# Kernel tuning notes

Measured on AMD Instinct MI355X. Metric: run time of the kernel, lower is better.

The kernel has to match this reference:

```python
import jax, jax.numpy as jnp
import numpy as np

N = 50000
E = 800000
IN_DIM = 128
HIDDEN = 32
HEADS = 4
NUM_CLASSES = 10


def _glorot(key, shape):
    fan_in, fan_out = shape
    lim = float(np.sqrt(6.0 / (fan_in + fan_out)))
    return jax.random.uniform(key, shape, jnp.float32, -lim, lim)


def transformer_conv(x, src, dst, Wq, bq, Wk, bk, Wv, bv, Ws, bs, heads, out_ch, concat):
    """PyG TransformerConv (root_weight=True, beta=False, no edge_attr), eval mode."""
    n = x.shape[0]
    q = (x @ Wq + bq).reshape(n, heads, out_ch)
    k = (x @ Wk + bk).reshape(n, heads, out_ch)
    v = (x @ Wv + bv).reshape(n, heads, out_ch)
    # gather per-edge: query from target i, key/value from source j
    qe = q[dst]                                  # [E, H, C]
    ke = k[src]                                  # [E, H, C]
    ve = v[src]                                  # [E, H, C]
    logits = jnp.einsum('ehc,ehc->eh', qe, ke) / jnp.sqrt(jnp.float32(out_ch))
    # segment softmax over incoming edges of each target node
    m = jax.ops.segment_max(logits, dst, num_segments=n)        # [N, H]
    m = jnp.where(jnp.isfinite(m), m, 0.0)
    e = jnp.exp(logits - m[dst])                                # [E, H]
    denom = jax.ops.segment_sum(e, dst, num_segments=n)         # [N, H]
    alpha = e / (denom[dst] + 1e-16)                            # [E, H]
    agg = jax.ops.segment_sum(alpha[..., None] * ve, dst, num_segments=n)  # [N, H, C]
    if concat:
        out = agg.reshape(n, heads * out_ch)
    else:
        out = agg.mean(axis=1)
    return out + x @ Ws + bs  # root/skip connection


def setup_inputs() -> dict:
    key = jax.random.key(0)
    ks = jax.random.split(key, 20)
    x = jax.random.normal(ks[0], (N, IN_DIM), jnp.float32)
    edge_index = jax.random.randint(ks[1], (2, E), 0, N, jnp.int32)
    d1 = HEADS * HIDDEN  # conv1 per-head stacked width = 128
    params = {
        'Wq1': _glorot(ks[2], (IN_DIM, d1)), 'bq1': jnp.zeros((d1,), jnp.float32),
        'Wk1': _glorot(ks[3], (IN_DIM, d1)), 'bk1': jnp.zeros((d1,), jnp.float32),
        'Wv1': _glorot(ks[4], (IN_DIM, d1)), 'bv1': jnp.zeros((d1,), jnp.float32),
        'Ws1': _glorot(ks[5], (IN_DIM, d1)), 'bs1': jnp.zeros((d1,), jnp.float32),
        'Wq2': _glorot(ks[6], (d1, NUM_CLASSES)), 'bq2': jnp.zeros((NUM_CLASSES,), jnp.float32),
        'Wk2': _glorot(ks[7], (d1, NUM_CLASSES)), 'bk2': jnp.zeros((NUM_CLASSES,), jnp.float32),
        'Wv2': _glorot(ks[8], (d1, NUM_CLASSES)), 'bv2': jnp.zeros((NUM_CLASSES,), jnp.float32),
        'Ws2': _glorot(ks[9], (d1, NUM_CLASSES)), 'bs2': jnp.zeros((NUM_CLASSES,), jnp.float32),
    }
    return {'x': x, 'edge_index': edge_index, **params}


def reference(x, edge_index,
              Wq1, bq1, Wk1, bk1, Wv1, bv1, Ws1, bs1,
              Wq2, bq2, Wk2, bk2, Wv2, bv2, Ws2, bs2):
    src, dst = edge_index[0], edge_index[1]
    h = transformer_conv(x, src, dst, Wq1, bq1, Wk1, bk1, Wv1, bv1, Ws1, bs1,
                         HEADS, HIDDEN, concat=True)
    h = jax.nn.elu(h)
    # dropout is identity in eval mode
    out = transformer_conv(h, src, dst, Wq2, bq2, Wk2, bk2, Wv2, bv2, Ws2, bs2,
                           1, NUM_CLASSES, concat=False)
    return out
```

## Files before the change

kernel.cpp:

```cpp
#include <hip/hip_runtime.h>
#include <hip/hip_fp16.h>
#include <math.h>

#define NN 50000
#define EE 800000
#define NB 196
#define NBK 128
#define BKN 391
#define CH 4096

typedef _Float16 f16x8 __attribute__((ext_vector_type(8)));
typedef float f32x4 __attribute__((ext_vector_type(4)));
typedef float f32x2 __attribute__((ext_vector_type(2)));

__device__ inline float elu1(float x) { return x > 0.f ? x : expm1f(x); }

__global__ __launch_bounds__(256) void convert_x_deg(
    const float* __restrict__ x, __half* __restrict__ xh,
    const int* __restrict__ dst, int* __restrict__ deg)
{
    const int i = blockIdx.x * 256 + threadIdx.x;
    if (i < NN * 32) {
        const float4 v = ((const float4*)x)[i];
        ((__half2*)xh)[i * 2] = __floats2half2_rn(v.x, v.y);
        ((__half2*)xh)[i * 2 + 1] = __floats2half2_rn(v.z, v.w);
    }
    if (i < EE) atomicAdd(&deg[dst[i]], 1);
}

__global__ __launch_bounds__(256) void build_weights(
    const float* __restrict__ Wq, const float* __restrict__ Wk,
    const float* __restrict__ Wv, const float* __restrict__ Ws,
    const float* __restrict__ Wq2, const float* __restrict__ bq2,
    const float* __restrict__ Wk2, const float* __restrict__ bk2,
    const float* __restrict__ Wv2, const float* __restrict__ bv2,
    const float* __restrict__ Ws2, const float* __restrict__ bs2,
    __half* __restrict__ Wt, __half* __restrict__ W2t, float* __restrict__ bias2)
{
    const int idx = blockIdx.x * 256 + threadIdx.x;
    if (idx < 8192) {
        const int col = idx >> 7, k = idx & 127;
        const int m = col >> 4, j = col & 15;
        const float* W = m == 0 ? Wq2 : m == 1 ? Wk2 : m == 2 ? Wv2 : Ws2;
        W2t[idx] = (__half)(j < 10 ? W[k * 10 + j] : 0.f);
    }
    if (idx < 64) {
        const int m = idx >> 4, j = idx & 15;
        const float* b = m == 0 ? bq2 : m == 1 ? bk2 : m == 2 ? bv2 : bs2;
        bias2[idx] = j < 10 ? b[j] : 0.f;
    }
    __shared__ float tile[32][33];
    const int mat = blockIdx.x >> 4;
    const int tid = blockIdx.x & 15;
    const int k0 = (tid >> 2) * 32, c0 = (tid & 3) * 32;
    const float* W = mat == 0 ? Wq : mat == 1 ? Wk : mat == 2 ? Wv : Ws;
    const int r = threadIdx.x >> 5;
    const int c = threadIdx.x & 31;
    for (int rr = r; rr < 32; rr += 8) tile[rr][c] = W[(size_t)(k0 + rr) * 128 + c0 + c];
    __syncthreads();
    for (int rr = r; rr < 32; rr += 8)
        Wt[((size_t)mat * 128 + c0 + rr) * 128 + k0 + c] = (__half)tile[c][rr];
}

__global__ __launch_bounds__(256) void block_sums(
    const int* __restrict__ deg, int* __restrict__ bsum)
{
    __shared__ int ws[4];
    const int t = threadIdx.x;
    const int idx = blockIdx.x * 256 + t;
    int d = (idx < NN) ? deg[idx] : 0;
    #pragma unroll
    for (int off = 32; off; off >>= 1) d += __shfl_down(d, off, 64);
    if ((t & 63) == 0) ws[t >> 6] = d;
    __syncthreads();
    if (t == 0) bsum[blockIdx.x] = ws[0] + ws[1] + ws[2] + ws[3];
}

__global__ __launch_bounds__(256) void scan_bsums(int* __restrict__ bsum)
{
    __shared__ int s[256];
    const int t = threadIdx.x;
    int v = (t < NB) ? bsum[t] : 0;
    s[t] = v;
    __syncthreads();
    for (int off = 1; off < 256; off <<= 1) {
        int u = (t >= off) ? s[t - off] : 0;
        __syncthreads();
        s[t] += u;
        __syncthreads();
    }
    if (t < NB) bsum[t] = (t == 0) ? 0 : s[t - 1];
}

__global__ __launch_bounds__(256) void write_rowptr(
    const int* __restrict__ deg, const int* __restrict__ bsum,
    int* __restrict__ rowptr, int* __restrict__ bcur)
{
    __shared__ int s[256];
    const int t = threadIdx.x;
    const int idx = blockIdx.x * 256 + t;
    const int d = (idx < NN) ? deg[idx] : 0;
    s[t] = d;
    __syncthreads();
    for (int off = 1; off < 256; off <<= 1) {
        int u = (t >= off) ? s[t - off] : 0;
        __syncthreads();
        s[t] += u;
        __syncthreads();
    }
    const int excl = ((t == 0) ? 0 : s[t - 1]) + bsum[blockIdx.x];
    if (idx < NN) {
        rowptr[idx] = excl;
        if (idx % BKN == 0) bcur[idx / BKN] = excl;
    }
    if (idx == NN - 1) rowptr[NN] = excl + d;
}

__global__ __launch_bounds__(256) void bucket_stage(
    const int* __restrict__ src, const int* __restrict__ dst,
    int* __restrict__ bcur, unsigned* __restrict__ bpair)
{
    __shared__ unsigned ep[CH];
    __shared__ unsigned short eb[CH];
    __shared__ unsigned stg[CH];
    __shared__ int cnt[NBK], off[NBK], pos[NBK], gbase[NBK];
    const int t = threadIdx.x;
    const int e0 = blockIdx.x * CH;
    const int n = min(CH, EE - e0);
    if (t < NBK) cnt[t] = 0;
    __syncthreads();
    for (int i = t; i < n; i += 256) {
        const int s = src[e0 + i], d = dst[e0 + i];
        ep[i] = (unsigned)s | ((unsigned)d << 16);
        const int b = d / BKN;
        eb[i] = (unsigned short)b;
        atomicAdd(&cnt[b], 1);
    }
    __syncthreads();
    if (t == 0) {
        int run = 0;
        for (int b = 0; b < NBK; ++b) { off[b] = run; pos[b] = run; run += cnt[b]; }
    }
    __syncthreads();
    if (t < NBK && cnt[t] > 0) gbase[t] = atomicAdd(&bcur[t], cnt[t]);
    __syncthreads();
    for (int i = t; i < n; i += 256) {
        const int b = eb[i];
        const int p = atomicAdd(&pos[b], 1);
        stg[p] = ep[i];
    }
    __syncthreads();
    for (int i = t; i < n; i += 256) {
        int lo = 0, hi = NBK - 1;
        while (lo < hi) { const int mid = (lo + hi + 1) >> 1; if (off[mid] <= i) lo = mid; else hi = mid - 1; }
        bpair[gbase[lo] + (i - off[lo])] = stg[i];
    }
}

__global__ __launch_bounds__(256) void bucket_scatter(
    const unsigned* __restrict__ bpair, const int* __restrict__ rowptr,
    int* __restrict__ esrc)
{
    __shared__ int lcur[BKN];
    const int b = blockIdx.x;
    const int n0 = b * BKN;
    const int n1 = min(NN, n0 + BKN);
    const int nn = n1 - n0;
    const int t = threadIdx.x;
    for (int i = t; i < nn; i += 256) lcur[i] = rowptr[n0 + i];
    __syncthreads();
    const int ebeg = rowptr[n0];
    const int eend = rowptr[n1];
    for (int i = ebeg + t; i < eend; i += 256) {
        const unsigned p = bpair[i];
        const int s = (int)(p & 0xFFFFu);
        const int d = (int)(p >> 16);
        const int pos = atomicAdd(&lcur[d - n0], 1);
        esrc[pos] = s;
    }
}

__global__ __launch_bounds__(128) void gemm_l1_mfma(
    const __half* __restrict__ xh, const __half* __restrict__ Wt,
    const float* __restrict__ bq, const float* __restrict__ bk,
    const float* __restrict__ bv, const float* __restrict__ bs,
    __half* __restrict__ oqh, unsigned char* __restrict__ ok8,
    unsigned char* __restrict__ ov8, __half* __restrict__ osh)
{
    __shared__ __align__(16) unsigned char ldsraw[128 * 272];
    const int pair = blockIdx.y;
    const int t = threadIdx.x;
    const int wave = t >> 6;
    const int lane = t & 63;
    const int l = lane & 15;
    const int g = lane >> 4;
    const int brow0 = blockIdx.x * 128;
    const int wrow0 = brow0 + wave * 64;

    f16x8 xf[4][4];
    #pragma unroll
    for (int rt = 0; rt < 4; ++rt) {
        int arow = wrow0 + rt * 16 + l;
        if (arow >= NN) arow = NN - 1;
        #pragma unroll
        for (int kk = 0; kk < 4; ++kk)
            xf[rt][kk] = *(const f16x8*)((const _Float16*)xh + (size_t)arow * 128 + kk * 32 + g * 8);
    }

    for (int mi = 0; mi < 2; ++mi) {
        const int mat = pair * 2 + mi;
        const bool isfp8 = (mat == 1 || mat == 2);
        const float* b = mat == 0 ? bq : mat == 1 ? bk : mat == 2 ? bv : bs;
        const _Float16* wt = (const _Float16*)Wt + (size_t)mat * 128 * 128;

        f16x8 wf[4], wfn[4];
        #pragma unroll
        for (int kk = 0; kk < 4; ++kk)
            wf[kk] = *(const f16x8*)(wt + (size_t)l * 128 + kk * 32 + g * 8);

        for (int ct = 0; ct < 8; ++ct) {
            if (ct < 7) {
                const int ncol = (ct + 1) * 16 + l;
                #pragma unroll
                for (int kk = 0; kk < 4; ++kk)
                    wfn[kk] = *(const f16x8*)(wt + (size_t)ncol * 128 + kk * 32 + g * 8);
            }
            f32x4 acc[4];
            #pragma unroll
            for (int rt = 0; rt < 4; ++rt) acc[rt] = (f32x4){0.f, 0.f, 0.f, 0.f};
            #pragma unroll
            for (int kk = 0; kk < 4; ++kk)
                #pragma unroll
                for (int rt = 0; rt < 4; ++rt)
                    acc[rt] = __builtin_amdgcn_mfma_f32_16x16x32_f16(wf[kk], xf[rt][kk], acc[rt], 0, 0, 0);

            const int col0 = ct * 16 + g * 4;
            const float4 bias = *(const float4*)(b + col0);
            #pragma unroll
            for (int rt = 0; rt < 4; ++rt) {
                const int lrow = wave * 64 + rt * 16 + l;
                const float r0 = acc[rt][0] + bias.x;
                const float r1 = acc[rt][1] + bias.y;
                const float r2 = acc[rt][2] + bias.z;
                const float r3 = acc[rt][3] + bias.w;
                if (isfp8) {
                    int p = __builtin_amdgcn_cvt_pk_fp8_f32(r0, r1, 0, false);
                    p = __builtin_amdgcn_cvt_pk_fp8_f32(r2, r3, p, true);
                    *(int*)&ldsraw[lrow * 144 + col0] = p;
                } else {
                    __half2 h01 = __floats2half2_rn(r0, r1);
                    __half2 h23 = __floats2half2_rn(r2, r3);
                    uint2 u;
                    u.x = *(unsigned*)&h01;
                    u.y = *(unsigned*)&h23;
                    *(uint2*)&ldsraw[lrow * 272 + col0 * 2] = u;
                }
            }
            #pragma unroll
            for (int kk = 0; kk < 4; ++kk) wf[kk] = wfn[kk];
        }

        __syncthreads();
        if (isfp8) {
            unsigned char* o = (mat == 1) ? ok8 : ov8;
            #pragma unroll
            for (int i = 0; i < 8; ++i) {
                const int idx = i * 128 + t;
                const int row = idx >> 3;
                const int seg = idx & 7;
                const int grow = brow0 + row;
                if (grow < NN)
                    *(uint4*)(o + (size_t)grow * 128 + seg * 16) = *(const uint4*)&ldsraw[row * 144 + seg * 16];
            }
        } else {
            __half* o = (mat == 0) ? oqh : osh;
            #pragma unroll
            for (int i = 0; i < 16; ++i) {
                const int idx = i * 128 + t;
                const int row = idx >> 4;
                const int seg = idx & 15;
                const int grow = brow0 + row;
                if (grow < NN)
                    *(uint4*)(o + (size_t)grow * 128 + seg * 8) = *(const uint4*)&ldsraw[row * 272 + seg * 16];
            }
        }
        __syncthreads();
    }
}

__global__ __launch_bounds__(256) void node_attn1(
    const __half* __restrict__ q1, const unsigned char* __restrict__ k8,
    const unsigned char* __restrict__ v8,
    const int* __restrict__ rowptr, const int* __restrict__ esrc,
    const __half* __restrict__ skiph,
    __half* __restrict__ hb)
{
    const int t = threadIdx.x;
    const int d = blockIdx.x * 8 + (t >> 5);
    if (d >= NN) return;
    const int ch4 = (t & 31) << 2;

    const int beg = rowptr[d];
    const int end = rowptr[d + 1];

    float q0, q1v, q2, q3;
    {
        const __half2 qa = *(const __half2*)(q1 + (size_t)d * 128 + ch4);
        const __half2 qb = *(const __half2*)(q1 + (size_t)d * 128 + ch4 + 2);
        const float2 fa = __half22float2(qa);
        const float2 fb = __half22float2(qb);
        q0 = fa.x * 0.17677669529663687f;
        q1v = fa.y * 0.17677669529663687f;
        q2 = fb.x * 0.17677669529663687f;
        q3 = fb.y * 0.17677669529663687f;
    }

    f32x4 accA = {0.f, 0.f, 0.f, 0.f}, accB = {0.f, 0.f, 0.f, 0.f};
    float sA = 0.f, sB = 0.f;

    int i = beg;
    int sa = (i < end) ? esrc[i] : 0;
    int sb = (i + 1 < end) ? esrc[i + 1] : 0;
    unsigned kA = *(const unsigned*)(k8 + (size_t)sa * 128 + ch4);
    unsigned vA = *(const unsigned*)(v8 + (size_t)sa * 128 + ch4);
    unsigned kB = *(const unsigned*)(k8 + (size_t)sb * 128 + ch4);
    unsigned vB = *(const unsigned*)(v8 + (size_t)sb * 128 + ch4);

    while (i + 1 < end) {
        const int ni = i + 2;
        const int nsa = (ni < end) ? esrc[ni] : 0;
        const int nsb = (ni + 1 < end) ? esrc[ni + 1] : 0;
        const unsigned nkA = *(const unsigned*)(k8 + (size_t)nsa * 128 + ch4);
        const unsigned nvA = *(const unsigned*)(v8 + (size_t)nsa * 128 + ch4);
        const unsigned nkB = *(const unsigned*)(k8 + (size_t)nsb * 128 + ch4);
        const unsigned nvB = *(const unsigned*)(v8 + (size_t)nsb * 128 + ch4);

        const f32x2 kA01 = __builtin_amdgcn_cvt_pk_f32_fp8((int)kA, false);
        const f32x2 kA23 = __builtin_amdgcn_cvt_pk_f32_fp8((int)kA, true);
        const f32x2 kB01 = __builtin_amdgcn_cvt_pk_f32_fp8((int)kB, false);
        const f32x2 kB23 = __builtin_amdgcn_cvt_pk_f32_fp8((int)kB, true);

        float pA = q0 * kA01[0] + q1v * kA01[1] + q2 * kA23[0] + q3 * kA23[1];
        float pB = q0 * kB01[0] + q1v * kB01[1] + q2 * kB23[0] + q3 * kB23[1];
        pA += __shfl_xor(pA, 4, 8); pB += __shfl_xor(pB, 4, 8);
        pA += __shfl_xor(pA, 2, 8); pB += __shfl_xor(pB, 2, 8);
        pA += __shfl_xor(pA, 1, 8); pB += __shfl_xor(pB, 1, 8);

        const f32x2 vA01 = __builtin_amdgcn_cvt_pk_f32_fp8((int)vA, false);
        const f32x2 vA23 = __builtin_amdgcn_cvt_pk_f32_fp8((int)vA, true);
        const f32x2 vB01 = __builtin_amdgcn_cvt_pk_f32_fp8((int)vB, false);
        const f32x2 vB23 = __builtin_amdgcn_cvt_pk_f32_fp8((int)vB, true);

        const float exA = __expf(pA - 4.0f);
        accA[0] += exA * vA01[0];
        accA[1] += exA * vA01[1];
        accA[2] += exA * vA23[0];
        accA[3] += exA * vA23[1];
        sA += exA;

        const float exB = __expf(pB - 4.0f);
        accB[0] += exB * vB01[0];
        accB[1] += exB * vB01[1];
        accB[2] += exB * vB23[0];
        accB[3] += exB * vB23[1];
        sB += exB;

        kA = nkA; vA = nvA; kB = nkB; vB = nvB;
        i = ni;
    }
    if (i < end) {
        const f32x2 kA01 = __builtin_amdgcn_cvt_pk_f32_fp8((int)kA, false);
        const f32x2 kA23 = __builtin_amdgcn_cvt_pk_f32_fp8((int)kA, true);
        float pA = q0 * kA01[0] + q1v * kA01[1] + q2 * kA23[0] + q3 * kA23[1];
        pA += __shfl_xor(pA, 4, 8);
        pA += __shfl_xor(pA, 2, 8);
        pA += __shfl_xor(pA, 1, 8);
        const f32x2 vA01 = __builtin_amdgcn_cvt_pk_f32_fp8((int)vA, false);
        const f32x2 vA23 = __builtin_amdgcn_cvt_pk_f32_fp8((int)vA, true);
        const float exA = __expf(pA - 4.0f);
        accA[0] += exA * vA01[0];
        accA[1] += exA * vA01[1];
        accA[2] += exA * vA23[0];
        accA[3] += exA * vA23[1];
        sA += exA;
    }

    const float inv = 1.f / (sA + sB + 1e-16f);
    const __half2 sk01 = *(const __half2*)(skiph + (size_t)d * 128 + ch4);
    const __half2 sk23 = *(const __half2*)(skiph + (size_t)d * 128 + ch4 + 2);
    const float2 s01 = __half22float2(sk01);
    const float2 s23 = __half22float2(sk23);
    const float o0 = elu1(s01.x + (accA[0] + accB[0]) * inv);
    const float o1 = elu1(s01.y + (accA[1] + accB[1]) * inv);
    const float o2 = elu1(s23.x + (accA[2] + accB[2]) * inv);
    const float o3 = elu1(s23.y + (accA[3] + accB[3]) * inv);
    __half2 h01 = __floats2half2_rn(o0, o1);
    __half2 h23 = __floats2half2_rn(o2, o3);
    uint2 u;
    u.x = *(unsigned*)&h01;
    u.y = *(unsigned*)&h23;
    *(uint2*)(hb + (size_t)d * 128 + ch4) = u;
}

__global__ __launch_bounds__(128) void node_l2_mfma(
    const __half* __restrict__ hb, const __half* __restrict__ W2t,
    const float* __restrict__ bias2,
    __half* __restrict__ q2h, __half* __restrict__ kv2h,
    float* __restrict__ out)
{
    const int t = threadIdx.x;
    const int wave = t >> 6;
    const int lane = t & 63;
    const int l = lane & 15;
    const int g = lane >> 4;
    const int wrow0 = blockIdx.x * 128 + wave * 64;
    if (wrow0 >= NN) return;
    const bool full = (wrow0 + 64 <= NN);

    f16x8 hf[4][4];
    #pragma unroll
    for (int rt = 0; rt < 4; ++rt) {
        int arow = wrow0 + rt * 16 + l;
        if (!full && arow >= NN) arow = NN - 1;
        #pragma unroll
        for (int kk = 0; kk < 4; ++kk)
            hf[rt][kk] = *(const f16x8*)((const _Float16*)hb + (size_t)arow * 128 + kk * 32 + g * 8);
    }

    #pragma unroll
    for (int ct = 0; ct < 4; ++ct) {
        const int col = ct * 16 + l;
        f16x8 wf[4];
        #pragma unroll
        for (int kk = 0; kk < 4; ++kk)
            wf[kk] = *(const f16x8*)((const _Float16*)W2t + (size_t)col * 128 + kk * 32 + g * 8);

        f32x4 acc[4];
        #pragma unroll
        for (int rt = 0; rt < 4; ++rt) acc[rt] = (f32x4){0.f, 0.f, 0.f, 0.f};
        #pragma unroll
        for (int kk = 0; kk < 4; ++kk)
            #pragma unroll
            for (int rt = 0; rt < 4; ++rt)
                acc[rt] = __builtin_amdgcn_mfma_f32_16x16x32_f16(wf[kk], hf[rt][kk], acc[rt], 0, 0, 0);

        const int c0 = g * 4;
        const float4 bias = *(const float4*)(bias2 + ct * 16 + c0);
        #pragma unroll
        for (int rt = 0; rt < 4; ++rt) {
            const int row = wrow0 + rt * 16 + l;
            if (full || row < NN) {
                float4 r;
                r.x = acc[rt][0] + bias.x;
                r.y = acc[rt][1] + bias.y;
                r.z = acc[rt][2] + bias.z;
                r.w = acc[rt][3] + bias.w;
                if (ct == 3) {
                    if (g < 2) {
                        *(float4*)(out + (size_t)row * 10 + c0) = r;
                    } else if (g == 2) {
                        out[(size_t)row * 10 + 8] = r.x;
                        out[(size_t)row * 10 + 9] = r.y;
                    }
                } else {
                    __half* p = ct == 0 ? q2h + (size_t)row * 16 + c0
                              : kv2h + (size_t)row * 32 + (ct == 2 ? 16 : 0) + c0;
                    __half2 h01 = __floats2half2_rn(r.x, r.y);
                    __half2 h23 = __floats2half2_rn(r.z, r.w);
                    uint2 u;
                    u.x = *(unsigned*)&h01;
                    u.y = *(unsigned*)&h23;
                    *(uint2*)p = u;
                }
            }
        }
    }
}

__global__ __launch_bounds__(256) void node_attn2(
    const __half* __restrict__ q2h, const __half* __restrict__ kv2h,
    const int* __restrict__ rowptr, const int* __restrict__ esrc,
    float* __restrict__ out)
{
    const int t = threadIdx.x;
    const int d = blockIdx.x * 32 + (t >> 3);
    if (d >= NN) return;
    const int c = t & 7;
    const int beg = rowptr[d];
    const int end = rowptr[d + 1];

    float2 qv = __half22float2(*(const __half2*)(q2h + (size_t)d * 16 + 2 * c));
    qv.x *= 0.31622776601683794f;
    qv.y *= 0.31622776601683794f;

    float2 acc[4];
    float ss[4];
    #pragma unroll
    for (int j = 0; j < 4; ++j) { acc[j] = make_float2(0.f, 0.f); ss[j] = 0.f; }

    int i = beg;
    __half2 kr[4], vr[4];
    #pragma unroll
    for (int j = 0; j < 4; ++j) {
        const int s = (i + j < end) ? esrc[i + j] : 0;
        kr[j] = *(const __half2*)(kv2h + (size_t)s * 32 + 2 * c);
        vr[j] = *(const __half2*)(kv2h + (size_t)s * 32 + 16 + 2 * c);
    }

    while (i + 3 < end) {
        const int ni = i + 4;
        __half2 nk[4], nv[4];
        #pragma unroll
        for (int j = 0; j < 4; ++j) {
            const int s = (ni + j < end) ? esrc[ni + j] : 0;
            nk[j] = *(const __half2*)(kv2h + (size_t)s * 32 + 2 * c);
            nv[j] = *(const __half2*)(kv2h + (size_t)s * 32 + 16 + 2 * c);
        }
        #pragma unroll
        for (int j = 0; j < 4; ++j) {
            const float2 kf = __half22float2(kr[j]);
            const float2 vf = __half22float2(vr[j]);
            float p = qv.x * kf.x + qv.y * kf.y;
            p += __shfl_xor(p, 4, 8);
            p += __shfl_xor(p, 2, 8);
            p += __shfl_xor(p, 1, 8);
            const float ex = __expf(p - 2.0f);
            acc[j].x += ex * vf.x;
            acc[j].y += ex * vf.y;
            ss[j] += ex;
        }
        #pragma unroll
        for (int j = 0; j < 4; ++j) { kr[j] = nk[j]; vr[j] = nv[j]; }
        i = ni;
    }
    for (; i < end; ++i) {
        const int s = esrc[i];
        const float2 kf = __half22float2(*(const __half2*)(kv2h + (size_t)s * 32 + 2 * c));
        const float2 vf = __half22float2(*(const __half2*)(kv2h + (size_t)s * 32 + 16 + 2 * c));
        float p = qv.x * kf.x + qv.y * kf.y;
        p += __shfl_xor(p, 4, 8);
        p += __shfl_xor(p, 2, 8);
        p += __shfl_xor(p, 1, 8);
        const float ex = __expf(p - 2.0f);
        acc[0].x += ex * vf.x;
        acc[0].y += ex * vf.y;
        ss[0] += ex;
    }

    if (c < 5) {
        const float ssum = ss[0] + ss[1] + ss[2] + ss[3];
        const float inv = 1.f / (ssum + 1e-16f);
        float2 o = *(float2*)(out + (size_t)d * 10 + 2 * c);
        o.x += (acc[0].x + acc[1].x + acc[2].x + acc[3].x) * inv;
        o.y += (acc[0].y + acc[1].y + acc[2].y + acc[3].y) * inv;
        *(float2*)(out + (size_t)d * 10 + 2 * c) = o;
    }
}

extern "C" void kernel_launch(void* const* d_in, const int* in_sizes, int n_in,
                              void* d_out, int out_size, void* d_ws, size_t ws_size,
                              hipStream_t stream) {
    const float* x   = (const float*)d_in[0];
    const int*   ei  = (const int*)d_in[1];
    const float* Wq1 = (const float*)d_in[2];  const float* bq1 = (const float*)d_in[3];
    const float* Wk1 = (const float*)d_in[4];  const float* bk1 = (const float*)d_in[5];
    const float* Wv1 = (const float*)d_in[6];  const float* bv1 = (const float*)d_in[7];
    const float* Ws1 = (const float*)d_in[8];  const float* bs1 = (const float*)d_in[9];
    const float* Wq2 = (const float*)d_in[10]; const float* bq2 = (const float*)d_in[11];
    const float* Wk2 = (const float*)d_in[12]; const float* bk2 = (const float*)d_in[13];
    const float* Wv2 = (const float*)d_in[14]; const float* bv2 = (const float*)d_in[15];
    const float* Ws2 = (const float*)d_in[16]; const float* bs2 = (const float*)d_in[17];
    float* out = (float*)d_out;

    const int* src = ei;
    const int* dst = ei + EE;

    __half* xh    = (__half*)d_ws;
    __half* q1h   = xh + (size_t)NN * 128;
    __half* skiph = q1h + (size_t)NN * 128;
    __half* hb    = skiph + (size_t)NN * 128;
    unsigned char* k8 = (unsigned char*)(hb + (size_t)NN * 128);
    unsigned char* v8 = k8 + (size_t)NN * 128;
    __half* Wt    = (__half*)(v8 + (size_t)NN * 128);
    __half* W2t   = Wt + 4 * 128 * 128;
    __half* q2h   = W2t + 64 * 128;
    __half* kv2h  = q2h + (size_t)NN * 16;
    float* bias2  = (float*)(kv2h + (size_t)NN * 32);
    int* deg      = (int*)(bias2 + 64);
    int* rowptr   = deg + NN;
    int* bcur     = rowptr + NN + 1;
    int* bsum     = bcur + NBK;
    int* esrc     = bsum + NB;
    unsigned* bpair = (unsigned*)(esrc + EE);

    hipMemsetAsync(deg, 0, (size_t)NN * sizeof(int), stream);
    convert_x_deg<<<(NN * 32 + 255) / 256, 256, 0, stream>>>(x, xh, dst, deg);
    build_weights<<<64, 256, 0, stream>>>(Wq1, Wk1, Wv1, Ws1,
                                          Wq2, bq2, Wk2, bk2, Wv2, bv2, Ws2, bs2,
                                          Wt, W2t, bias2);

    block_sums<<<NB, 256, 0, stream>>>(deg, bsum);
    scan_bsums<<<1, 256, 0, stream>>>(bsum);
    write_rowptr<<<NB, 256, 0, stream>>>(deg, bsum, rowptr, bcur);
    bucket_stage<<<(EE + CH - 1) / CH, 256, 0, stream>>>(src, dst, bcur, bpair);
    bucket_scatter<<<NBK, 256, 0, stream>>>(bpair, rowptr, esrc);

    gemm_l1_mfma<<<dim3((NN + 127) / 128, 2), 128, 0, stream>>>(
        xh, Wt, bq1, bk1, bv1, bs1, q1h, k8, v8, skiph);

    node_attn1<<<(NN + 7) / 8, 256, 0, stream>>>(q1h, k8, v8, rowptr, esrc, skiph, hb);

    node_l2_mfma<<<(NN + 127) / 128, 128, 0, stream>>>(hb, W2t, bias2, q2h, kv2h, out);

    node_attn2<<<(NN + 31) / 32, 256, 0, stream>>>(q2h, kv2h, rowptr, esrc, out);
}
```

Baseline: 186.6 us.

## Rebalance layer-1 GEMM to 4 waves and narrow layer-2 attention to 4 lanes per node

The layer-1 projection GEMM now runs 256 threads per block, with each wave covering 32 rows instead of 64. This halves per-wave register use for the x fragments and accumulators, trading it for more weight-fragment reloads per row. The layer-2 attention kernel now assigns 4 lanes per destination node instead of 8, with each lane handling 4 channels via 8-byte loads. It processes two edges per iteration with prefetch, which reduces shuffle steps and idle lanes. The node_l2 output stores are also rewritten as float2 stores for alignment, since the 10-float row stride breaks float4 alignment.

After: 202.9 us. 8.7% more time.

```diff
diff --git a/kernel.cpp b/kernel.cpp
--- a/kernel.cpp
+++ b/kernel.cpp
@@ -180,7 +180,7 @@
     }
 }
 
-__global__ __launch_bounds__(128) void gemm_l1_mfma(
+__global__ __launch_bounds__(256) void gemm_l1_mfma(
     const __half* __restrict__ xh, const __half* __restrict__ Wt,
     const float* __restrict__ bq, const float* __restrict__ bk,
     const float* __restrict__ bv, const float* __restrict__ bs,
@@ -195,11 +195,11 @@
     const int l = lane & 15;
     const int g = lane >> 4;
     const int brow0 = blockIdx.x * 128;
-    const int wrow0 = brow0 + wave * 64;
-
-    f16x8 xf[4][4];
+    const int wrow0 = brow0 + wave * 32;
+
+    f16x8 xf[2][4];
     #pragma unroll
-    for (int rt = 0; rt < 4; ++rt) {
+    for (int rt = 0; rt < 2; ++rt) {
         int arow = wrow0 + rt * 16 + l;
         if (arow >= NN) arow = NN - 1;
         #pragma unroll
@@ -225,20 +225,20 @@
                 for (int kk = 0; kk < 4; ++kk)
                     wfn[kk] = *(const f16x8*)(wt + (size_t)ncol * 128 + kk * 32 + g * 8);
             }
-            f32x4 acc[4];
+            f32x4 acc[2];
             #pragma unroll
-            for (int rt = 0; rt < 4; ++rt) acc[rt] = (f32x4){0.f, 0.f, 0.f, 0.f};
+            for (int rt = 0; rt < 2; ++rt) acc[rt] = (f32x4){0.f, 0.f, 0.f, 0.f};
             #pragma unroll
             for (int kk = 0; kk < 4; ++kk)
                 #pragma unroll
-                for (int rt = 0; rt < 4; ++rt)
+                for (int rt = 0; rt < 2; ++rt)
                     acc[rt] = __builtin_amdgcn_mfma_f32_16x16x32_f16(wf[kk], xf[rt][kk], acc[rt], 0, 0, 0);
 
             const int col0 = ct * 16 + g * 4;
             const float4 bias = *(const float4*)(b + col0);
             #pragma unroll
-            for (int rt = 0; rt < 4; ++rt) {
-                const int lrow = wave * 64 + rt * 16 + l;
+            for (int rt = 0; rt < 2; ++rt) {
+                const int lrow = wave * 32 + rt * 16 + l;
                 const float r0 = acc[rt][0] + bias.x;
                 const float r1 = acc[rt][1] + bias.y;
                 const float r2 = acc[rt][2] + bias.z;
@@ -264,8 +264,8 @@
         if (isfp8) {
             unsigned char* o = (mat == 1) ? ok8 : ov8;
             #pragma unroll
-            for (int i = 0; i < 8; ++i) {
-                const int idx = i * 128 + t;
+            for (int i = 0; i < 4; ++i) {
+                const int idx = i * 256 + t;
                 const int row = idx >> 3;
                 const int seg = idx & 7;
                 const int grow = brow0 + row;
@@ -275,8 +275,8 @@
         } else {
             __half* o = (mat == 0) ? oqh : osh;
             #pragma unroll
-            for (int i = 0; i < 16; ++i) {
-                const int idx = i * 128 + t;
+            for (int i = 0; i < 8; ++i) {
+                const int idx = i * 256 + t;
                 const int row = idx >> 4;
                 const int seg = idx & 15;
                 const int grow = brow0 + row;
@@ -457,10 +457,10 @@
                 r.w = acc[rt][3] + bias.w;
                 if (ct == 3) {
                     if (g < 2) {
-                        *(float4*)(out + (size_t)row * 10 + c0) = r;
+                        *(float2*)(out + (size_t)row * 10 + c0) = make_float2(r.x, r.y);
+                        *(float2*)(out + (size_t)row * 10 + c0 + 2) = make_float2(r.z, r.w);
                     } else if (g == 2) {
-                        out[(size_t)row * 10 + 8] = r.x;
-                        out[(size_t)row * 10 + 9] = r.y;
+                        *(float2*)(out + (size_t)row * 10 + 8) = make_float2(r.x, r.y);
                     }
                 } else {
                     __half* p = ct == 0 ? q2h + (size_t)row * 16 + c0
@@ -483,77 +483,108 @@
     float* __restrict__ out)
 {
     const int t = threadIdx.x;
-    const int d = blockIdx.x * 32 + (t >> 3);
+    const int d = blockIdx.x * 64 + (t >> 2);
     if (d >= NN) return;
-    const int c = t & 7;
+    const int c = t & 3;
+    const int ch4 = c << 2;
     const int beg = rowptr[d];
     const int end = rowptr[d + 1];
 
-    float2 qv = __half22float2(*(const __half2*)(q2h + (size_t)d * 16 + 2 * c));
-    qv.x *= 0.31622776601683794f;
-    qv.y *= 0.31622776601683794f;
-
-    float2 acc[4];
-    float ss[4];
-    #pragma unroll
-    for (int j = 0; j < 4; ++j) { acc[j] = make_float2(0.f, 0.f); ss[j] = 0.f; }
+    float q0, q1v, q2v, q3v;
+    {
+        const __half2 qa = *(const __half2*)(q2h + (size_t)d * 16 + ch4);
+        const __half2 qb = *(const __half2*)(q2h + (size_t)d * 16 + ch4 + 2);
+        const float2 fa = __half22float2(qa);
+        const float2 fb = __half22float2(qb);
+        q0 = fa.x * 0.31622776601683794f;
+        q1v = fa.y * 0.31622776601683794f;
+        q2v = fb.x * 0.31622776601683794f;
+        q3v = fb.y * 0.31622776601683794f;
+    }
+
+    f32x4 accA = {0.f, 0.f, 0.f, 0.f}, accB = {0.f, 0.f, 0.f, 0.f};
+    float sA = 0.f, sB = 0.f;
 
     int i = beg;
-    __half2 kr[4], vr[4];
-    #pragma unroll
-    for (int j = 0; j < 4; ++j) {
-        const int s = (i + j < end) ? esrc[i + j] : 0;
-        kr[j] = *(const __half2*)(kv2h + (size_t)s * 32 + 2 * c);
-        vr[j] = *(const __half2*)(kv2h + (size_t)s * 32 + 16 + 2 * c);
-    }
-
-    while (i + 3 < end) {
-        const int ni = i + 4;
-        __half2 nk[4], nv[4];
-        #pragma unroll
-        for (int j = 0; j < 4; ++j) {
-            const int s = (ni + j < end) ? esrc[ni + j] : 0;
-            nk[j] = *(const __half2*)(kv2h + (size_t)s * 32 + 2 * c);
-            nv[j] = *(const __half2*)(kv2h + (size_t)s * 32 + 16 + 2 * c);
-        }
-        #pragma unroll
-        for (int j = 0; j < 4; ++j) {
-            const float2 kf = __half22float2(kr[j]);
-            const float2 vf = __half22float2(vr[j]);
-            float p = qv.x * kf.x + qv.y * kf.y;
-            p += __shfl_xor(p, 4, 8);
-            p += __shfl_xor(p, 2, 8);
-            p += __shfl_xor(p, 1, 8);
-            const float ex = __expf(p - 2.0f);
-            acc[j].x += ex * vf.x;
-            acc[j].y += ex * vf.y;
-            ss[j] += ex;
-        }
-        #pragma unroll
-        for (int j = 0; j < 4; ++j) { kr[j] = nk[j]; vr[j] = nv[j]; }
+    int sa = (i < end) ? esrc[i] : 0;
+    int sb = (i + 1 < end) ? esrc[i + 1] : 0;
+    uint2 kA = *(const uint2*)(kv2h + (size_t)sa * 32 + ch4);
+    uint2 vA = *(const uint2*)(kv2h + (size_t)sa * 32 + 16 + ch4);
+    uint2 kB = *(const uint2*)(kv2h + (size_t)sb * 32 + ch4);
+    uint2 vB = *(const uint2*)(kv2h + (size_t)sb * 32 + 16 + ch4);
+
+    while (i + 1 < end) {
+        const int ni = i + 2;
+        const int nsa = (ni < end) ? esrc[ni] : 0;
+        const int nsb = (ni + 1 < end) ? esrc[ni + 1] : 0;
+        const uint2 nkA = *(const uint2*)(kv2h + (size_t)nsa * 32 + ch4);
+        const uint2 nvA = *(const uint2*)(kv2h + (size_t)nsa * 32 + 16 + ch4);
+        const uint2 nkB = *(const uint2*)(kv2h + (size_t)nsb * 32 + ch4);
+        const uint2 nvB = *(const uint2*)(kv2h + (size_t)nsb * 32 + 16 + ch4);
+
+        const float2 kA01 = __half22float2(*(const __half2*)&kA.x);
+        const float2 kA23 = __half22float2(*(const __half2*)&kA.y);
+        const float2 kB01 = __half22float2(*(const __half2*)&kB.x);
+        const float2 kB23 = __half22float2(*(const __half2*)&kB.y);
+
+        float pA = q0 * kA01.x + q1v * kA01.y + q2v * kA23.x + q3v * kA23.y;
+        float pB = q0 * kB01.x + q1v * kB01.y + q2v * kB23.x + q3v * kB23.y;
+        pA += __shfl_xor(pA, 2, 4); pB += __shfl_xor(pB, 2, 4);
+        pA += __shfl_xor(pA, 1, 4); pB += __shfl_xor(pB, 1, 4);
+
+        const float2 vA01 = __half22float2(*(const __half2*)&vA.x);
+        const float2 vA23 = __half22float2(*(const __half2*)&vA.y);
+        const float2 vB01 = __half22float2(*(const __half2*)&vB.x);
+        const float2 vB23 = __half22float2(*(const __half2*)&vB.y);
+
+        const float exA = __expf(pA - 2.0f);
+        accA[0] += exA * vA01.x;
+        accA[1] += exA * vA01.y;
+        accA[2] += exA * vA23.x;
+        accA[3] += exA * vA23.y;
+        sA += exA;
+
+        const float exB = __expf(pB - 2.0f);
+        accB[0] += exB * vB01.x;
+        accB[1] += exB * vB01.y;
+        accB[2] += exB * vB23.x;
+        accB[3] += exB * vB23.y;
+        sB += exB;
+
+        kA = nkA; vA = nvA; kB = nkB; vB = nvB;
         i = ni;
     }
-    for (; i < end; ++i) {
-        const int s = esrc[i];
-        const float2 kf = __half22float2(*(const __half2*)(kv2h + (size_t)s * 32 + 2 * c));
-        const float2 vf = __half22float2(*(const __half2*)(kv2h + (size_t)s * 32 + 16 + 2 * c));
-        float p = qv.x * kf.x + qv.y * kf.y;
-        p += __shfl_xor(p, 4, 8);
-        p += __shfl_xor(p, 2, 8);
-        p += __shfl_xor(p, 1, 8);
-        const float ex = __expf(p - 2.0f);
-        acc[0].x += ex * vf.x;
-        acc[0].y += ex * vf.y;
-        ss[0] += ex;
-    }
-
-    if (c < 5) {
-        const float ssum = ss[0] + ss[1] + ss[2] + ss[3];
-        const float inv = 1.f / (ssum + 1e-16f);
-        float2 o = *(float2*)(out + (size_t)d * 10 + 2 * c);
-        o.x += (acc[0].x + acc[1].x + acc[2].x + acc[3].x) * inv;
-        o.y += (acc[0].y + acc[1].y + acc[2].y + acc[3].y) * inv;
-        *(float2*)(out + (size_t)d * 10 + 2 * c) = o;
+    if (i < end) {
+        const float2 kA01 = __half22float2(*(const __half2*)&kA.x);
+        const float2 kA23 = __half22float2(*(const __half2*)&kA.y);
+        float pA = q0 * kA01.x + q1v * kA01.y + q2v * kA23.x + q3v * kA23.y;
+        pA += __shfl_xor(pA, 2, 4);
+        pA += __shfl_xor(pA, 1, 4);
+        const float2 vA01 = __half22float2(*(const __half2*)&vA.x);
+        const float2 vA23 = __half22float2(*(const __half2*)&vA.y);
+        const float exA = __expf(pA - 2.0f);
+        accA[0] += exA * vA01.x;
+        accA[1] += exA * vA01.y;
+        accA[2] += exA * vA23.x;
+        accA[3] += exA * vA23.y;
+        sA += exA;
+    }
+
+    const float inv = 1.f / (sA + sB + 1e-16f);
+    if (c < 2) {
+        float2 o0 = *(float2*)(out + (size_t)d * 10 + ch4);
+        float2 o1 = *(float2*)(out + (size_t)d * 10 + ch4 + 2);
+        o0.x += (accA[0] + accB[0]) * inv;
+        o0.y += (accA[1] + accB[1]) * inv;
+        o1.x += (accA[2] + accB[2]) * inv;
+        o1.y += (accA[3] + accB[3]) * inv;
+        *(float2*)(out + (size_t)d * 10 + ch4) = o0;
+        *(float2*)(out + (size_t)d * 10 + ch4 + 2) = o1;
+    } else if (c == 2) {
+        float2 o0 = *(float2*)(out + (size_t)d * 10 + 8);
+        o0.x += (accA[0] + accB[0]) * inv;
+        o0.y += (accA[1] + accB[1]) * inv;
+        *(float2*)(out + (size_t)d * 10 + 8) = o0;
     }
 }
 
@@ -605,12 +636,12 @@
     bucket_stage<<<(EE + CH - 1) / CH, 256, 0, stream>>>(src, dst, bcur, bpair);
     bucket_scatter<<<NBK, 256, 0, stream>>>(bpair, rowptr, esrc);
 
-    gemm_l1_mfma<<<dim3((NN + 127) / 128, 2), 128, 0, stream>>>(
+    gemm_l1_mfma<<<dim3((NN + 127) / 128, 2), 256, 0, stream>>>(
         xh, Wt, bq1, bk1, bv1, bs1, q1h, k8, v8, skiph);
 
     node_attn1<<<(NN + 7) / 8, 256, 0, stream>>>(q1h, k8, v8, rowptr, esrc, skiph, hb);
 
     node_l2_mfma<<<(NN + 127) / 128, 128, 0, stream>>>(hb, W2t, bias2, q2h, kv2h, out);
 
-    node_attn2<<<(NN + 31) / 32, 256, 0, stream>>>(q2h, kv2h, rowptr, esrc, out);
-}
+    node_attn2<<<(NN + 63) / 64, 256, 0, stream>>>(q2h, kv2h, rowptr, esrc, out);
+}
```
